# Performance work log

Hardware: AMD Instinct MI355X
Metric: run time of the kernel (lower is better)

Reference implementation:

```python
import jax, jax.numpy as jnp
import numpy as np


def setup_inputs() -> dict:
    key = jax.random.key(0)
    k1, k2 = jax.random.split(key)
    B, Tx, C, Ty, d = 16, 128, 64, 128, 768
    xs = jax.random.normal(k1, (B, Tx, d), dtype=jnp.float32)
    ys = jax.random.normal(k2, (B, C, Ty, d), dtype=jnp.float32)
    return {"xs": xs, "ys": ys}


def reference(xs, ys):
    # scores[b,t,c,s] = xs[b,t,:] . ys[b,c,s,:]
    scores = jnp.einsum("btd,bcsd->btcs", xs, ys)  # (B,Tx,C,Ty)
    # hard attention: max over candidate tokens, sum over query tokens
    return scores.max(axis=-1).sum(axis=1)  # (B,C)
```

## Files before the change

### kernel.cpp

```cpp
#include <hip/hip_runtime.h>


typedef __attribute__((ext_vector_type(8))) short short8;
typedef __attribute__((ext_vector_type(4))) float floatx4;

#define B_DIM 16
#define TX 128
#define CC 64
#define TY 128
#define DD 768
#define KITERS (DD / 32)

__device__ __forceinline__ short f2bf(float f) {
  unsigned u = __builtin_bit_cast(unsigned, f);
  u += 0x7FFFu + ((u >> 16) & 1u);
  return (short)(u >> 16);
}

__device__ __forceinline__ floatx4 ntload4(const float* p) {
  return __builtin_nontemporal_load(reinterpret_cast<const floatx4*>(p));
}

__global__ __launch_bounds__(256) void cvt_xs(const float* __restrict__ xs,
                                              short* __restrict__ xb, int n4) {
  int i = blockIdx.x * blockDim.x + threadIdx.x;
  if (i >= n4) return;
  float4 v = reinterpret_cast<const float4*>(xs)[i];
  short4 o;
  o.x = f2bf(v.x);
  o.y = f2bf(v.y);
  o.z = f2bf(v.z);
  o.w = f2bf(v.w);
  reinterpret_cast<short4*>(xb)[i] = o;
}

__global__ __launch_bounds__(256, 2) void hardattn(const short* __restrict__ xb,
                                                   const float* __restrict__ ys,
                                                   float* __restrict__ out) {
  const int blk = blockIdx.x;
  const int b = blk >> 6;
  const int tid = threadIdx.x;
  const int w = tid >> 6;
  const int lane = tid & 63;
  const int l16 = lane & 15;
  const int kg = lane >> 4;

  const float* Bp = ys + (size_t)blk * TY * DD;

  floatx4 acc[8][2];
#pragma unroll
  for (int mt = 0; mt < 8; mt++)
#pragma unroll
    for (int nt = 0; nt < 2; nt++) acc[mt][nt] = (floatx4)0.f;

  const short* aBase = xb + (size_t)b * TX * DD + (size_t)l16 * DD + kg * 8;
  const float* bBase0 = Bp + (size_t)(w * 32 + l16) * DD + kg * 8;
  const float* bBase1 = bBase0 + (size_t)16 * DD;

  short8 abuf[2][8];
  floatx4 bbuf[2][4];

  bbuf[0][0] = ntload4(bBase0);
  bbuf[0][1] = ntload4(bBase0 + 4);
  bbuf[0][2] = ntload4(bBase1);
  bbuf[0][3] = ntload4(bBase1 + 4);
#pragma unroll
  for (int mt = 0; mt < 8; mt++)
    abuf[0][mt] = *reinterpret_cast<const short8*>(aBase + (size_t)mt * 16 * DD);

#pragma unroll
  for (int it = 0; it < KITERS; it++) {
    const int cur = it & 1;
    const int nxt = cur ^ 1;
    if (it + 1 < KITERS) {
      const int kn = (it + 1) * 32;
      bbuf[nxt][0] = ntload4(bBase0 + kn);
      bbuf[nxt][1] = ntload4(bBase0 + kn + 4);
      bbuf[nxt][2] = ntload4(bBase1 + kn);
      bbuf[nxt][3] = ntload4(bBase1 + kn + 4);
#pragma unroll
      for (int mt = 0; mt < 8; mt++)
        abuf[nxt][mt] =
            *reinterpret_cast<const short8*>(aBase + (size_t)mt * 16 * DD + kn);
    }

    short8 bf0, bf1;
#pragma unroll
    for (int j = 0; j < 4; j++) {
      bf0[j] = f2bf(bbuf[cur][0][j]);
      bf0[j + 4] = f2bf(bbuf[cur][1][j]);
      bf1[j] = f2bf(bbuf[cur][2][j]);
      bf1[j + 4] = f2bf(bbuf[cur][3][j]);
    }

#pragma unroll
    for (int mt = 0; mt < 8; mt++) {
      acc[mt][0] =
          __builtin_amdgcn_mfma_f32_16x16x32_bf16(abuf[cur][mt], bf0, acc[mt][0], 0, 0, 0);
      acc[mt][1] =
          __builtin_amdgcn_mfma_f32_16x16x32_bf16(abuf[cur][mt], bf1, acc[mt][1], 0, 0, 0);
    }
  }

  __shared__ float part[4][TX];
  __shared__ float wsum[2];

#pragma unroll
  for (int mt = 0; mt < 8; mt++) {
#pragma unroll
    for (int r = 0; r < 4; r++) {
      float v = fmaxf(acc[mt][0][r], acc[mt][1][r]);
      v = fmaxf(v, __shfl_xor(v, 1, 64));
      v = fmaxf(v, __shfl_xor(v, 2, 64));
      v = fmaxf(v, __shfl_xor(v, 4, 64));
      v = fmaxf(v, __shfl_xor(v, 8, 64));
      if (l16 == 0) part[w][mt * 16 + kg * 4 + r] = v;
    }
  }
  __syncthreads();

  if (tid < 128) {
    float rm = fmaxf(fmaxf(part[0][tid], part[1][tid]),
                     fmaxf(part[2][tid], part[3][tid]));
    float s = rm;
    s += __shfl_down(s, 32, 64);
    s += __shfl_down(s, 16, 64);
    s += __shfl_down(s, 8, 64);
    s += __shfl_down(s, 4, 64);
    s += __shfl_down(s, 2, 64);
    s += __shfl_down(s, 1, 64);
    if (lane == 0) wsum[w] = s;
  }
  __syncthreads();
  if (tid == 0) out[blk] = wsum[0] + wsum[1];
}

extern "C" void kernel_launch(void* const* d_in, const int* in_sizes, int n_in,
                              void* d_out, int out_size, void* d_ws, size_t ws_size,
                              hipStream_t stream) {
  const float* xs = (const float*)d_in[0];
  const float* ys = (const float*)d_in[1];
  float* out = (float*)d_out;

  const size_t xs_elems = (size_t)B_DIM * TX * DD;
  short* xb = (short*)d_ws;
  int n4 = (int)(xs_elems / 4);
  cvt_xs<<<(n4 + 255) / 256, 256, 0, stream>>>(xs, xb, n4);
  hardattn<<<B_DIM * CC, 256, 0, stream>>>(xb, ys, out);
}
```

Measured before the change: 684.4 us.

## Stage ys tiles through LDS with async global_load_lds double buffering

```diff
diff --git a/kernel.cpp b/kernel.cpp
--- a/kernel.cpp
+++ b/kernel.cpp
@@ -1,4 +1,5 @@
 #include <hip/hip_runtime.h>
+#include <stdint.h>
 
 
 typedef __attribute__((ext_vector_type(8))) short short8;
@@ -9,16 +10,13 @@
 #define CC 64
 #define TY 128
 #define DD 768
-#define KITERS (DD / 32)
+#define BK 32
+#define KITERS (DD / BK)
 
 __device__ __forceinline__ short f2bf(float f) {
   unsigned u = __builtin_bit_cast(unsigned, f);
   u += 0x7FFFu + ((u >> 16) & 1u);
   return (short)(u >> 16);
-}
-
-__device__ __forceinline__ floatx4 ntload4(const float* p) {
-  return __builtin_nontemporal_load(reinterpret_cast<const floatx4*>(p));
 }
 
 __global__ __launch_bounds__(256) void cvt_xs(const float* __restrict__ xs,
@@ -34,9 +32,13 @@
   reinterpret_cast<short4*>(xb)[i] = o;
 }
 
-__global__ __launch_bounds__(256, 2) void hardattn(const short* __restrict__ xb,
+__global__ __launch_bounds__(256, 3) void hardattn(const short* __restrict__ xb,
                                                    const float* __restrict__ ys,
                                                    float* __restrict__ out) {
+  __shared__ float bstage[2][TY * BK];
+  __shared__ float part[4][TX];
+  __shared__ float wsum[2];
+
   const int blk = blockIdx.x;
   const int b = blk >> 6;
   const int tid = threadIdx.x;
@@ -47,6 +49,21 @@
 
   const float* Bp = ys + (size_t)blk * TY * DD;
 
+  const int srow = (w << 5) + (lane >> 3);
+  const int gchunk = (lane & 7) ^ (srow & 7);
+  const float* gsrc = Bp + (size_t)srow * DD + gchunk * 4;
+
+#define STAGE(bufidx, k0)                                                  \
+  {                                                                        \
+    _Pragma("unroll") for (int j = 0; j < 4; j++) {                        \
+      const float* g = gsrc + (size_t)(8 * j) * DD + (k0);                 \
+      float* l = &bstage[bufidx][((w << 5) + 8 * j) * BK];                 \
+      __builtin_amdgcn_global_load_lds(                                    \
+          (const __attribute__((address_space(1))) void*)g,                \
+          (__attribute__((address_space(3))) void*)l, 16, 0, 0);           \
+    }                                                                      \
+  }
+
   floatx4 acc[8][2];
 #pragma unroll
   for (int mt = 0; mt < 8; mt++)
@@ -54,56 +71,47 @@
     for (int nt = 0; nt < 2; nt++) acc[mt][nt] = (floatx4)0.f;
 
   const short* aBase = xb + (size_t)b * TX * DD + (size_t)l16 * DD + kg * 8;
-  const float* bBase0 = Bp + (size_t)(w * 32 + l16) * DD + kg * 8;
-  const float* bBase1 = bBase0 + (size_t)16 * DD;
 
-  short8 abuf[2][8];
-  floatx4 bbuf[2][4];
+  const int p0 = ((kg << 1) ^ (l16 & 7)) * 4;
+  const int p1 = (((kg << 1) | 1) ^ (l16 & 7)) * 4;
+  const int rb0 = ((w << 5) + l16) * BK;
+  const int rb1 = ((w << 5) + 16 + l16) * BK;
 
-  bbuf[0][0] = ntload4(bBase0);
-  bbuf[0][1] = ntload4(bBase0 + 4);
-  bbuf[0][2] = ntload4(bBase1);
-  bbuf[0][3] = ntload4(bBase1 + 4);
+  STAGE(0, 0);
+
+  for (int it = 0; it < KITERS; it++) {
+    __syncthreads();
+    const int cur = it & 1;
+    if (it + 1 < KITERS) STAGE(cur ^ 1, (it + 1) * BK);
+    const int k0 = it * BK;
+
+    short8 a[8];
 #pragma unroll
-  for (int mt = 0; mt < 8; mt++)
-    abuf[0][mt] = *reinterpret_cast<const short8*>(aBase + (size_t)mt * 16 * DD);
+    for (int mt = 0; mt < 8; mt++)
+      a[mt] = *reinterpret_cast<const short8*>(aBase + (size_t)mt * 16 * DD + k0);
 
-#pragma unroll
-  for (int it = 0; it < KITERS; it++) {
-    const int cur = it & 1;
-    const int nxt = cur ^ 1;
-    if (it + 1 < KITERS) {
-      const int kn = (it + 1) * 32;
-      bbuf[nxt][0] = ntload4(bBase0 + kn);
-      bbuf[nxt][1] = ntload4(bBase0 + kn + 4);
-      bbuf[nxt][2] = ntload4(bBase1 + kn);
-      bbuf[nxt][3] = ntload4(bBase1 + kn + 4);
-#pragma unroll
-      for (int mt = 0; mt < 8; mt++)
-        abuf[nxt][mt] =
-            *reinterpret_cast<const short8*>(aBase + (size_t)mt * 16 * DD + kn);
-    }
-
+    const float* rb = &bstage[cur][0];
+    floatx4 c00 = *reinterpret_cast<const floatx4*>(rb + rb0 + p0);
+    floatx4 c01 = *reinterpret_cast<const floatx4*>(rb + rb0 + p1);
+    floatx4 c10 = *reinterpret_cast<const floatx4*>(rb + rb1 + p0);
+    floatx4 c11 = *reinterpret_cast<const floatx4*>(rb + rb1 + p1);
     short8 bf0, bf1;
 #pragma unroll
     for (int j = 0; j < 4; j++) {
-      bf0[j] = f2bf(bbuf[cur][0][j]);
-      bf0[j + 4] = f2bf(bbuf[cur][1][j]);
-      bf1[j] = f2bf(bbuf[cur][2][j]);
-      bf1[j + 4] = f2bf(bbuf[cur][3][j]);
+      bf0[j] = f2bf(c00[j]);
+      bf0[j + 4] = f2bf(c01[j]);
+      bf1[j] = f2bf(c10[j]);
+      bf1[j + 4] = f2bf(c11[j]);
     }
 
 #pragma unroll
     for (int mt = 0; mt < 8; mt++) {
       acc[mt][0] =
-          __builtin_amdgcn_mfma_f32_16x16x32_bf16(abuf[cur][mt], bf0, acc[mt][0], 0, 0, 0);
+          __builtin_amdgcn_mfma_f32_16x16x32_bf16(a[mt], bf0, acc[mt][0], 0, 0, 0);
       acc[mt][1] =
-          __builtin_amdgcn_mfma_f32_16x16x32_bf16(abuf[cur][mt], bf1, acc[mt][1], 0, 0, 0);
+          __builtin_amdgcn_mfma_f32_16x16x32_bf16(a[mt], bf1, acc[mt][1], 0, 0, 0);
     }
   }
-
-  __shared__ float part[4][TX];
-  __shared__ float wsum[2];
 
 #pragma unroll
   for (int mt = 0; mt < 8; mt++) {
```

After: 559.4 us. 18.3% less time.
